# Kernel optimization log

Measured on AMD Instinct MI355X. Metric: run time of the kernel, lower is better.

The kernel has to match this reference:

```python
import jax, jax.numpy as jnp
import numpy as np

# ---------------- config (from ObjectDetector source) ----------------
B = 2; IMG = 224; STRIDE = 32; FH = IMG // STRIDE          # 7x7 feature map
C_FEAT = 1024
SIZES = (32., 64., 128., 256., 512.); RATIOS = (0.5, 1.0, 2.0)
A = len(SIZES) * len(RATIOS)                                # 15 anchors/loc
NA = FH * FH * A                                            # 735 anchors/img
PRE_NMS = min(1000, NA); POST_NMS = min(1000, NA)           # testing config
RPN_NMS_T = 0.7; RPN_MIN_SIZE = 1e-3
NUM_CLASSES = 37
ROI_OUT = 7; ROI_SR = 2; ROI_SCALE = 1.0 / STRIDE
REP = 1024
SCORE_T = 0.05; DET_NMS_T = 0.5; DETS_PER_IMG = 100
CAND_K = 2048            # candidate cap before final batched NMS
MIN_SIZE_DET = 1e-2
BBOX_CLIP = float(np.log(1000.0 / 16.0))


def make_anchors():
    scales = np.array(SIZES, np.float32); ratios = np.array(RATIOS, np.float32)
    h_r = np.sqrt(ratios); w_r = 1.0 / h_r
    ws = (w_r[:, None] * scales[None, :]).reshape(-1)
    hs = (h_r[:, None] * scales[None, :]).reshape(-1)
    base = np.round(np.stack([-ws, -hs, ws, hs], 1) / 2.0)   # [A,4]
    sy, sx = np.meshgrid(np.arange(FH) * STRIDE, np.arange(FH) * STRIDE, indexing='ij')
    shifts = np.stack([sx.reshape(-1), sy.reshape(-1), sx.reshape(-1), sy.reshape(-1)], 1).astype(np.float32)
    return jnp.asarray((shifts[:, None, :] + base[None, :, :]).reshape(-1, 4))  # [NA,4] (H,W,A)


def conv(x, w, b, stride=1, pad=0):
    y = jax.lax.conv_general_dilated(x, w, (stride, stride), [(pad, pad)] * 2,
                                     dimension_numbers=('NCHW', 'OIHW', 'NCHW'))
    return y + b[None, :, None, None]


def decode_boxes(deltas, boxes, weights):
    wx, wy, ww, wh = weights
    w = boxes[..., 2] - boxes[..., 0]; h = boxes[..., 3] - boxes[..., 1]
    cx = boxes[..., 0] + 0.5 * w; cy = boxes[..., 1] + 0.5 * h
    dx = deltas[..., 0] / wx; dy = deltas[..., 1] / wy
    dw = jnp.minimum(deltas[..., 2] / ww, BBOX_CLIP)
    dh = jnp.minimum(deltas[..., 3] / wh, BBOX_CLIP)
    pcx = dx * w + cx; pcy = dy * h + cy
    pw = jnp.exp(dw) * w; ph = jnp.exp(dh) * h
    return jnp.stack([pcx - 0.5 * pw, pcy - 0.5 * ph, pcx + 0.5 * pw, pcy + 0.5 * ph], -1)


def clip_boxes(b):
    x = jnp.clip(b[..., 0::2], 0.0, float(IMG)); y = jnp.clip(b[..., 1::2], 0.0, float(IMG))
    return jnp.stack([x[..., 0], y[..., 0], x[..., 1], y[..., 1]], -1)


def box_iou(a, b):
    area_a = (a[:, 2] - a[:, 0]) * (a[:, 3] - a[:, 1])
    area_b = (b[:, 2] - b[:, 0]) * (b[:, 3] - b[:, 1])
    lt = jnp.maximum(a[:, None, :2], b[None, :, :2])
    rb = jnp.minimum(a[:, None, 2:], b[None, :, 2:])
    wh = jnp.clip(rb - lt, 0.0, None)
    inter = wh[..., 0] * wh[..., 1]
    return inter / jnp.maximum(area_a[:, None] + area_b[None, :] - inter, 1e-9)


def nms_keep(boxes, scores, thresh):
    """Greedy NMS; returns keep mask in original order (fixed shapes)."""
    n = boxes.shape[0]
    order = jnp.argsort(-scores)
    iou = box_iou(*(jax.lax.stop_gradient(boxes[order]),) * 2)
    idx = jnp.arange(n)
    def body(i, keep):
        sup = (iou[i] > thresh) & (idx > i) & keep[i]
        return keep & ~sup
    keep_sorted = jax.lax.fori_loop(0, n, body, jnp.ones(n, bool))
    return jnp.zeros(n, bool).at[order].set(keep_sorted)


def rpn_filter_one(obj_logits, deltas, anchors):
    # obj_logits [NA], deltas [NA,4] (detached, as in torchvision RPN)
    top_v, top_i = jax.lax.top_k(obj_logits, PRE_NMS)
    boxes = clip_boxes(decode_boxes(deltas[top_i], anchors[top_i], (1., 1., 1., 1.)))
    prob = jax.nn.sigmoid(top_v)
    ws = boxes[:, 2] - boxes[:, 0]; hs = boxes[:, 3] - boxes[:, 1]
    prob = jnp.where((ws >= RPN_MIN_SIZE) & (hs >= RPN_MIN_SIZE), prob, -1.0)
    prob = jnp.where(nms_keep(boxes, prob, RPN_NMS_T), prob, -1.0)
    sv, si = jax.lax.top_k(prob, POST_NMS)
    return boxes[si], sv > 0.0


def bilinear(f_hwc, ys, xs):
    # torchvision roi_align bilinear sampling; f_hwc [H,W,C], ys/xs [R,O]
    H, W, _ = f_hwc.shape
    vy = (ys >= -1.0) & (ys <= H); vx = (xs >= -1.0) & (xs <= W)
    y = jnp.clip(ys, 0.0, None); x = jnp.clip(xs, 0.0, None)
    y0 = jnp.minimum(jnp.floor(y).astype(jnp.int32), H - 1)
    x0 = jnp.minimum(jnp.floor(x).astype(jnp.int32), W - 1)
    y1 = jnp.minimum(y0 + 1, H - 1); x1 = jnp.minimum(x0 + 1, W - 1)
    y = jnp.where(y0 == H - 1, y0.astype(y.dtype), y)
    x = jnp.where(x0 == W - 1, x0.astype(x.dtype), x)
    ly = y - y0; lx = x - x0; hy = 1.0 - ly; hx = 1.0 - lx
    g = lambda yi, xi: f_hwc[yi[:, :, None], xi[:, None, :]]   # [R,O,O,C]
    val = ((hy[:, :, None] * hx[:, None, :])[..., None] * g(y0, x0)
         + (hy[:, :, None] * lx[:, None, :])[..., None] * g(y0, x1)
         + (ly[:, :, None] * hx[:, None, :])[..., None] * g(y1, x0)
         + (ly[:, :, None] * lx[:, None, :])[..., None] * g(y1, x1))
    return val * (vy[:, :, None] & vx[:, None, :])[..., None]


def roi_align_one(feat_chw, rois):
    # feat [C,H,W], rois [R,4] -> [R,C,7,7]; output_size=7, sampling_ratio=2, scale=1/32
    f = jnp.transpose(feat_chw, (1, 2, 0))
    x1 = rois[:, 0] * ROI_SCALE; y1 = rois[:, 1] * ROI_SCALE
    rw = jnp.maximum(rois[:, 2] * ROI_SCALE - x1, 1.0)
    rh = jnp.maximum(rois[:, 3] * ROI_SCALE - y1, 1.0)
    bw = rw / ROI_OUT; bh = rh / ROI_OUT
    grid = jnp.arange(ROI_OUT, dtype=jnp.float32)
    acc = 0.0
    for iy in range(ROI_SR):
        ys = y1[:, None] + (grid[None, :] + (iy + 0.5) / ROI_SR) * bh[:, None]
        for ix in range(ROI_SR):
            xs = x1[:, None] + (grid[None, :] + (ix + 0.5) / ROI_SR) * bw[:, None]
            acc = acc + bilinear(f, ys, xs)
    return jnp.transpose(acc / (ROI_SR * ROI_SR), (0, 3, 1, 2))


def postprocess_one(logits, box_deltas, proposals, roi_valid):
    R = logits.shape[0]
    scores = jax.nn.softmax(logits, -1)
    boxes = clip_boxes(decode_boxes(box_deltas.reshape(R, NUM_CLASSES, 4),
                                    proposals[:, None, :], (10., 10., 5., 5.)))
    boxes = boxes[:, 1:, :].reshape(-1, 4)       # drop background class
    scores = jnp.where(roi_valid[:, None], scores[:, 1:], 0.0).reshape(-1)
    labels = jnp.broadcast_to(jnp.arange(1, NUM_CLASSES)[None, :], (R, NUM_CLASSES - 1)).reshape(-1)
    ws = boxes[:, 2] - boxes[:, 0]; hs = boxes[:, 3] - boxes[:, 1]
    ok = (ws >= MIN_SIZE_DET) & (hs >= MIN_SIZE_DET) & (scores > SCORE_T)
    cs, ci = jax.lax.top_k(jnp.where(ok, scores, -1.0), CAND_K)
    cb = boxes[ci]; cl = labels[ci]
    off = cl.astype(cb.dtype) * (IMG + 1.0)      # batched (per-class) NMS trick
    keep = nms_keep(cb + off[:, None], cs, DET_NMS_T)
    tv, ti = jax.lax.top_k(jnp.where(keep, cs, -1.0), DETS_PER_IMG)
    valid = tv > 0.0
    out_boxes = jnp.where(valid[:, None], cb[ti], 0.0)
    out_scores = jnp.where(valid, tv, 0.0)
    out_labels = jnp.where(valid, cl[ti], 0).astype(out_boxes.dtype)
    return jnp.concatenate([out_boxes, out_scores[:, None], out_labels[:, None]], -1)  # [100,6]


def forward(images, params, anchors):
    (bb_w, bb_b, rpn_w, rpn_b, cls_w, cls_b, reg_w, reg_b,
     fc1_w, fc1_b, fc2_w, fc2_b, clsp_w, clsp_b, boxp_w, boxp_b) = params
    Bn = images.shape[0]
    feats = jax.nn.relu(conv(images, bb_w, bb_b, stride=STRIDE))        # [B,1024,7,7]
    t = jax.nn.relu(conv(feats, rpn_w, rpn_b, stride=1, pad=1))
    obj = jnp.transpose(conv(t, cls_w, cls_b), (0, 2, 3, 1)).reshape(Bn, -1)            # [B,NA]
    reg = jnp.transpose(conv(t, reg_w, reg_b).reshape(Bn, A, 4, FH, FH),
                        (0, 3, 4, 1, 2)).reshape(Bn, -1, 4)                              # [B,NA,4]
    obj_d = jax.lax.stop_gradient(obj); reg_d = jax.lax.stop_gradient(reg)  # RPN detaches
    proposals, roi_valid = jax.vmap(lambda o, d: rpn_filter_one(o, d, anchors))(obj_d, reg_d)
    pooled = jax.vmap(roi_align_one)(feats, proposals)                  # [B,R,1024,7,7]
    x = pooled.reshape(Bn * POST_NMS, -1)
    x = jax.nn.relu(x @ fc1_w.T + fc1_b)
    x = jax.nn.relu(x @ fc2_w.T + fc2_b)
    logits = (x @ clsp_w.T + clsp_b).reshape(Bn, POST_NMS, NUM_CLASSES)
    bdelt = (x @ boxp_w.T + boxp_b).reshape(Bn, POST_NMS, NUM_CLASSES * 4)
    return jax.vmap(postprocess_one)(logits, bdelt, proposals, roi_valid)  # [B,100,6]


def setup_inputs() -> dict:
    key = jax.random.key(0)
    ks = jax.random.split(key, 10)
    w = lambda k, shape, s=0.02: jax.random.normal(k, shape, jnp.float32) * s
    return {
        'images': jax.random.uniform(ks[0], (B, 1, IMG, IMG), jnp.float32),
        'bb_w': w(ks[1], (C_FEAT, 1, STRIDE, STRIDE)), 'bb_b': jnp.zeros((C_FEAT,), jnp.float32),
        'rpn_w': w(ks[2], (C_FEAT, C_FEAT, 3, 3)), 'rpn_b': jnp.zeros((C_FEAT,), jnp.float32),
        'cls_w': w(ks[3], (A, C_FEAT, 1, 1)), 'cls_b': jnp.zeros((A,), jnp.float32),
        'reg_w': w(ks[4], (4 * A, C_FEAT, 1, 1)), 'reg_b': jnp.zeros((4 * A,), jnp.float32),
        'fc1_w': w(ks[5], (REP, C_FEAT * ROI_OUT * ROI_OUT), 0.005), 'fc1_b': jnp.zeros((REP,), jnp.float32),
        'fc2_w': w(ks[6], (REP, REP)), 'fc2_b': jnp.zeros((REP,), jnp.float32),
        'clsp_w': w(ks[7], (NUM_CLASSES, REP)), 'clsp_b': jnp.zeros((NUM_CLASSES,), jnp.float32),
        'boxp_w': w(ks[8], (NUM_CLASSES * 4, REP)), 'boxp_b': jnp.zeros((NUM_CLASSES * 4,), jnp.float32),
    }


def reference(images, bb_w, bb_b, rpn_w, rpn_b, cls_w, cls_b, reg_w, reg_b,
              fc1_w, fc1_b, fc2_w, fc2_b, clsp_w, clsp_b, boxp_w, boxp_b):
    anchors = make_anchors()
    params = (bb_w, bb_b, rpn_w, rpn_b, cls_w, cls_b, reg_w, reg_b,
              fc1_w, fc1_b, fc2_w, fc2_b, clsp_w, clsp_b, boxp_w, boxp_b)
    return forward(images, params, anchors)
```

## Files before the change

### kernel.cpp

```cpp
#include <hip/hip_runtime.h>
#include <math.h>

#define NANCH 735
#define NCAND 26460
#define NCANDP 26624
#define BBCLIP 4.135166556742356f
#define KF1 4864
#define KHALF 2432
#define MROW 768
#define MTOT 1536

typedef short bf16x8 __attribute__((ext_vector_type(8)));
typedef float f32x4 __attribute__((ext_vector_type(4)));

__device__ __forceinline__ unsigned short f2b(float f) {
  unsigned int u = __float_as_uint(f);
  unsigned int r = (u >> 16) & 1u;
  u += 0x7fffu + r;
  return (unsigned short)(u >> 16);
}

__device__ __forceinline__ void anchor_of(int i, float* o) {
  int pos = i / 15, a = i % 15;
  int iy = pos / 7, ix = pos % 7;
// ... 1 lines not shown
  double ratio = (rr == 0) ? 0.5 : (rr == 1 ? 1.0 : 2.0);
  double scale = (double)(32 << sc);
  double hr = sqrt(ratio), wr = 1.0 / hr;
  double wsz = wr * scale, hsz = hr * scale;
  float bx1 = (float)rint(-wsz * 0.5), by1 = (float)rint(-hsz * 0.5);
  float bx2 = (float)rint(wsz * 0.5),  by2 = (float)rint(hsz * 0.5);
  float sx = (float)(ix * 32), sy = (float)(iy * 32);
  o[0] = sx + bx1; o[1] = sy + by1; o[2] = sx + bx2; o[3] = sy + by2;
}

__device__ __forceinline__ bool before_(float va, int ia, float vb, int ib) {
  return (va > vb) || (va == vb && ia < ib);
}

template<int NTOT, int NTH>
__device__ void bitonic_sort_sh(float* v, int* id) {
  const int t = threadIdx.x;
  for (int k = 2; k <= NTOT; k <<= 1) {
    for (int j = k >> 1; j > 0; j >>= 1) {
      for (int s = t; s < NTOT; s += NTH) {
        int p = s ^ j;
        if (p > s) {
          float v1 = v[s], v2 = v[p];
          int i1 = id[s], i2 = id[p];
          bool up = ((s & k) == 0);
          if (before_(v2, i2, v1, i1) == up) {
            v[s] = v2; id[s] = i2; v[p] = v1; id[p] = i1;
          }
        }
      }
      __syncthreads();
    }
  }
}

template<int NTOT, int NTH>
__device__ void bitonic_merge_sh(float* v, int* id) {
  const int t = threadIdx.x;
  for (int j = NTOT >> 1; j > 0; j >>= 1) {
    for (int s = t; s < NTOT; s += NTH) {
      int p = s ^ j;
      if (p > s) {
        float v1 = v[s], v2 = v[p];
        int i1 = id[s], i2 = id[p];
        if (before_(v2, i2, v1, i1)) {
          v[s] = v2; id[s] = i2; v[p] = v1; id[p] = i1;
        }
      }
    }
    __syncthreads();
  }
}

__global__ void k_im2col_bb(const float* __restrict__ images, unsigned short* __restrict__ patch) {
  int i = blockIdx.x * 256 + threadIdx.x;
  if (i >= 98 * 1024) return;
  int rowi = i >> 10, k = i & 1023;
  int b = rowi / 49, pos = rowi % 49;
  int oy = pos / 7, ox = pos % 7;
  int ky = k >> 5, kx = k & 31;
  patch[i] = f2b(images[((size_t)b * 224 + oy * 32 + ky) * 224 + ox * 32 + kx]);
}

__global__ void k_im2col_rpn(const unsigned short* __restrict__ bbh,
                             unsigned short* __restrict__ im2) {
  int i = blockIdx.x * 256 + threadIdx.x;
  if (i >= 98 * 9216) return;
  int rowi = i / 9216, k = i % 9216;
  int b = rowi / 49, pos = rowi % 49;
  int oy = pos / 7, ox = pos % 7;
  int ic = k / 9, kk = k % 9;
  int ky = kk / 3, kx = kk % 3;
  int y = oy + ky - 1, x = ox + kx - 1;
  unsigned short v = 0;
  if ((unsigned)y < 7u && (unsigned)x < 7u)
    v = bbh[((size_t)(b * 49 + y * 7 + x)) * 1024 + ic];
  im2[i] = v;
}

__global__ __launch_bounds__(256) void k_gemm_bf16(
    const unsigned short* __restrict__ A, int lda, int M,
    const unsigned short* __restrict__ B, int ldb,
    float* __restrict__ P, int N, int Kchunk,
    const int* __restrict__ nvalid, int Msplit, int boff)
{
  __shared__ __attribute__((aligned(16))) unsigned short As[2][128][40];
  __shared__ __attribute__((aligned(16))) unsigned short Bs[2][128][40];
  const int G = gridDim.x * gridDim.y * gridDim.z;
  int lid = blockIdx.x + gridDim.x * (blockIdx.y + gridDim.y * blockIdx.z);
  lid = (lid & 7) * (G >> 3) + (lid >> 3);
  const int bx = lid % gridDim.x;
  const int rest = lid / gridDim.x;
  const int by = rest % gridDim.y, bz = rest / gridDim.y;
  const int m0 = bx * 128, n0 = by * 128;
  if (nvalid) {
    int img = (Msplit && m0 >= Msplit) ? 1 : 0;
    int lm = m0 - img * Msplit;
    if (lm >= nvalid[img]) return;
    B += (size_t)img * boff;
  }
  const int t = threadIdx.x;
  const int lane = t & 63, wid = t >> 6;
  const int wm = (wid >> 1) * 64, wn = (wid & 1) * 64;
  const size_t k0 = (size_t)bz * Kchunk;
  f32x4 acc[4][4];
#pragma unroll
  for (int i = 0; i < 4; ++i)
#pragma unroll
    for (int j = 0; j < 4; ++j) acc[i][j] = (f32x4){0.f, 0.f, 0.f, 0.f};
  const int r0 = t >> 2, c0 = (t & 3) * 8;
  const int fr = lane & 15, fk = (lane >> 4) * 8;
  const int gmA0 = m0 + r0, gmA1 = m0 + r0 + 64;
  const bool vA0 = gmA0 < M, vA1 = gmA1 < M;
  const unsigned short* pA0 = A + (size_t)gmA0 * lda + k0 + c0;
  const unsigned short* pA1 = A + (size_t)gmA1 * lda + k0 + c0;
  const unsigned short* pB0 = B + (size_t)(n0 + r0) * ldb + k0 + c0;
  const unsigned short* pB1 = B + (size_t)(n0 + r0 + 64) * ldb + k0 + c0;
  bf16x8 rA0 = {}, rA1 = {}, rB0, rB1;
  if (vA0) rA0 = *(const bf16x8*)pA0;
  if (vA1) rA1 = *(const bf16x8*)pA1;
  rB0 = *(const bf16x8*)pB0;
  rB1 = *(const bf16x8*)pB1;
  const int nt = Kchunk >> 5;
  int cur = 0;
  for (int it = 0; it < nt; ++it) {
    *(bf16x8*)&As[cur][r0][c0] = rA0;
    *(bf16x8*)&As[cur][r0 + 64][c0] = rA1;
    *(bf16x8*)&Bs[cur][r0][c0] = rB0;
    *(bf16x8*)&Bs[cur][r0 + 64][c0] = rB1;
    __syncthreads();
    if (it + 1 < nt) {
      size_t ofs = (size_t)(it + 1) * 32;
      rA0 = vA0 ? *(const bf16x8*)(pA0 + ofs) : (bf16x8){};
      rA1 = vA1 ? *(const bf16x8*)(pA1 + ofs) : (bf16x8){};
      rB0 = *(const bf16x8*)(pB0 + ofs);
      rB1 = *(const bf16x8*)(pB1 + ofs);
    }
    bf16x8 af[4], bg[4];
#pragma unroll
    for (int i = 0; i < 4; ++i) af[i] = *(const bf16x8*)&As[cur][wm + i * 16 + fr][fk];
#pragma unroll
    for (int j = 0; j < 4; ++j) bg[j] = *(const bf16x8*)&Bs[cur][wn + j * 16 + fr][fk];
#pragma unroll
    for (int i = 0; i < 4; ++i)
#pragma unroll
      for (int j = 0; j < 4; ++j)
        acc[i][j] = __builtin_amdgcn_mfma_f32_16x16x32_bf16(af[i], bg[j], acc[i][j], 0, 0, 0);
    cur ^= 1;
  }
  float* Pp = P + (size_t)bz * M * N;
#pragma unroll
  for (int i = 0; i < 4; ++i) {
#pragma unroll
    for (int r = 0; r < 4; ++r) {
      int gm = m0 + wm + i * 16 + (lane >> 4) * 4 + r;
      if (gm < M) {
#pragma unroll
        for (int j = 0; j < 4; ++j)
          Pp[(size_t)gm * N + n0 + wn + j * 16 + (lane & 15)] = acc[i][j][r];
      }
    }
  }
}

__global__ __launch_bounds__(256) void k_gemm_mb(
    const unsigned short* __restrict__ A,
    const unsigned short* __restrict__ W1p,
    unsigned short* __restrict__ Bmat)
{
  __shared__ __attribute__((aligned(16))) unsigned short As[2][128][40];
  __shared__ __attribute__((aligned(16))) unsigned short Bs[2][128][40];
  __shared__ unsigned short tile[98][130];
  const int G = gridDim.x * gridDim.y * gridDim.z;
  int lid = blockIdx.x + gridDim.x * (blockIdx.y + gridDim.y * blockIdx.z);
  lid = (lid & 7) * (G >> 3) + (lid >> 3);
  const int rest = lid;
  const int by = rest % gridDim.y, p = rest / gridDim.y;
  const int n0 = by * 128;
  const int M = 98;
  const unsigned short* B = W1p + (size_t)p * 1048576;
  const int t = threadIdx.x;
  const int lane = t & 63, wid = t >> 6;
  const int wm = (wid >> 1) * 64, wn = (wid & 1) * 64;
  f32x4 acc[4][4];
#pragma unroll
  for (int i = 0; i < 4; ++i)
#pragma unroll
    for (int j = 0; j < 4; ++j) acc[i][j] = (f32x4){0.f, 0.f, 0.f, 0.f};
  const int r0 = t >> 2, c0 = (t & 3) * 8;
  const int fr = lane & 15, fk = (lane >> 4) * 8;
  int gA0 = r0; if (gA0 >= M) gA0 = M - 1;
  int gA1 = r0 + 64; if (gA1 >= M) gA1 = M - 1;
  const unsigned short* pA0 = A + (size_t)gA0 * 1024 + c0;
  const unsigned short* pA1 = A + (size_t)gA1 * 1024 + c0;
  const unsigned short* pB0 = B + (size_t)(n0 + r0) * 1024 + c0;
  const unsigned short* pB1 = B + (size_t)(n0 + r0 + 64) * 1024 + c0;
  bf16x8 rA0 = *(const bf16x8*)pA0;
  bf16x8 rA1 = *(const bf16x8*)pA1;
  bf16x8 rB0 = *(const bf16x8*)pB0;
  bf16x8 rB1 = *(const bf16x8*)pB1;
  const int nt = 1024 >> 5;
  int cur = 0;
  for (int it = 0; it < nt; ++it) {
    *(bf16x8*)&As[cur][r0][c0] = rA0;
    *(bf16x8*)&As[cur][r0 + 64][c0] = rA1;
    *(bf16x8*)&Bs[cur][r0][c0] = rB0;
    *(bf16x8*)&Bs[cur][r0 + 64][c0] = rB1;
    __syncthreads();
    if (it + 1 < nt) {
      size_t ofs = (size_t)(it + 1) * 32;
      rA0 = *(const bf16x8*)(pA0 + ofs);
      rA1 = *(const bf16x8*)(pA1 + ofs);
      rB0 = *(const bf16x8*)(pB0 + ofs);
      rB1 = *(const bf16x8*)(pB1 + ofs);
    }
    bf16x8 af[4], bg[4];
#pragma unroll
    for (int i = 0; i < 4; ++i) af[i] = *(const bf16x8*)&As[cur][wm + i * 16 + fr][fk];
#pragma unroll
    for (int j = 0; j < 4; ++j) bg[j] = *(const bf16x8*)&Bs[cur][wn + j * 16 + fr][fk];
#pragma unroll
    for (int i = 0; i < 4; ++i)
#pragma unroll
      for (int j = 0; j < 4; ++j)
        acc[i][j] = __builtin_amdgcn_mfma_f32_16x16x32_bf16(af[i], bg[j], acc[i][j], 0, 0, 0);
    cur ^= 1;
  }
  __syncthreads();
#pragma unroll
  for (int i = 0; i < 4; ++i) {
#pragma unroll
    for (int r = 0; r < 4; ++r) {
      int gm = wm + i * 16 + (lane >> 4) * 4 + r;
      if (gm < M) {
#pragma unroll
        for (int j = 0; j < 4; ++j)
          tile[gm][wn + j * 16 + (lane & 15)] = f2b(acc[i][j][r]);
      }
    }
  }
  __syncthreads();
  {
    int nl = t >> 1, b2 = t & 1;
    unsigned short* dst = Bmat + (size_t)(n0 + nl) * KF1 + b2 * KHALF + p * 49;
    for (int qq = 0; qq < 49; ++qq) dst[qq] = tile[b2 * 49 + qq][nl];
  }
  if (p == 0) {
// ... 16 lines not shown
  int t = threadIdx.x;
  for (int j = t; j < KHALF; j += 256) g[j] = 0.f;
  __syncthreads();
  if (t < 49) {
    int pr = b * NANCH + r; if (pr > 2 * NANCH - 1) pr = 2 * NANCH - 1;
    const float* roi = props + (size_t)pr * 4;
    int p = t, oy = p / 7, ox = p % 7;
    float x1 = roi[0] * 0.03125f, y1 = roi[1] * 0.03125f;
    float rw = fmaxf(roi[2] * 0.03125f - x1, 1.f);
    float rh = fmaxf(roi[3] * 0.03125f - y1, 1.f);
    float bw = rw / 7.f, bh = rh / 7.f;
    float* gb = g + p * 49;
    for (int iy = 0; iy < 2; ++iy) {
      for (int ix = 0; ix < 2; ++ix) {
        float ys = y1 + ((float)oy + ((float)iy + 0.5f) * 0.5f) * bh;
        float xs = x1 + ((float)ox + ((float)ix + 0.5f) * 0.5f) * bw;
        bool vy = (ys >= -1.f) && (ys <= 7.f);
        bool vx = (xs >= -1.f) && (xs <= 7.f);
        float yc = fmaxf(ys, 0.f), xc = fmaxf(xs, 0.f);
        int y0 = min(max((int)floorf(yc), 0), 6), x0 = min(max((int)floorf(xc), 0), 6);
        int y1i = min(y0 + 1, 6), x1i = min(x0 + 1, 6);
        if (y0 == 6) yc = 6.f;
        if (x0 == 6) xc = 6.f;
        float ly = yc - (float)y0, lx = xc - (float)x0;
        float hy = 1.f - ly, hx = 1.f - lx;
        float vm = (vy && vx) ? 0.25f : 0.f;
        gb[y0 * 7 + x0]   += hy * hx * vm;
        gb[y0 * 7 + x1i]  += hy * lx * vm;
        gb[y1i * 7 + x0]  += ly * hx * vm;
        gb[y1i * 7 + x1i] += ly * lx * vm;
      }
    }
  }
  __syncthreads();
  unsigned short* Gr = Gmat + (size_t)rg * KHALF;
  for (int j = t; j < KHALF; j += 256) Gr[j] = f2b(g[j]);
}

__global__ void k_reduce(const float* __restrict__ P, float* __restrict__ dst,
                         unsigned short* __restrict__ dst16,
                         int S, int M, int N, const float* __restrict__ bias, int flags)
{
  size_t i = (size_t)blockIdx.x * 256 + threadIdx.x;
  size_t tot = (size_t)M * N;
  if (i >= tot) return;
  float v = (flags & 1) ? 0.f : dst[i];
  for (int s = 0; s < S; ++s) v += P[(size_t)s * tot + i];
  if (flags & 2) v += bias[i % (size_t)N];
  if (flags & 4) v = fmaxf(v, 0.f);
  if (!(flags & 16)) dst[i] = v;
  if (flags & 8) dst16[i] = f2b(v);
}

__global__ void k_f2b3(const float* __restrict__ s1, unsigned short* __restrict__ d1,
                       const float* __restrict__ s2, unsigned short* __restrict__ d2,
                       const float* __restrict__ s3, unsigned short* __restrict__ d3,
                       const float* __restrict__ cw, const float* __restrict__ bw,
                       unsigned short* __restrict__ d4)
{
  int i = (blockIdx.x * 256 + threadIdx.x) * 4;
  const float* s; unsigned short* d; int off;
  if (i < 1048576) { s = s1; d = d1; off = i; }
  else if (i < 2097152) { s = s2; d = d2; off = i - 1048576; }
  else if (i < 11534336) { s = s3; d = d3; off = i - 2097152; }
  else if (i < 11796480) {
    int off4 = i - 11534336;
    int row = off4 >> 10, col = off4 & 1023;
    ushort4 o;
    if (row < 37) {
      float4 v = *(const float4*)(cw + (size_t)row * 1024 + col);
      o.x = f2b(v.x); o.y = f2b(v.y); o.z = f2b(v.z); o.w = f2b(v.w);
    } else if (row < 185) {
      float4 v = *(const float4*)(bw + (size_t)(row - 37) * 1024 + col);
      o.x = f2b(v.x); o.y = f2b(v.y); o.z = f2b(v.z); o.w = f2b(v.w);
    } else {
      o.x = 0; o.y = 0; o.z = 0; o.w = 0;
    }
    *(ushort4*)(d4 + off4) = o;
    return;
  }
  else return;
  float4 v = *(const float4*)(s + off);
  ushort4 o;
  o.x = f2b(v.x); o.y = f2b(v.y); o.z = f2b(v.z); o.w = f2b(v.w);
  *(ushort4*)(d + off) = o;
}

__global__ __launch_bounds__(256) void k_w1perm2(const float* __restrict__ w,
                                                 unsigned short* __restrict__ o)
{
  __shared__ unsigned short tile[128 * 50];
  const int n = blockIdx.x, ct = blockIdx.y;
  const float* src = w + (size_t)n * 50176 + (size_t)ct * 128 * 49;
  const int t = threadIdx.x;
  for (int i = t; i < 6272; i += 256) {
    int cl = i / 49, p = i % 49;
    tile[cl * 50 + p] = f2b(src[i]);
  }
  __syncthreads();
  for (int j = t; j < 6272; j += 256) {
    int p = j >> 7, cl = j & 127;
    o[((size_t)p * 1024 + n) * 1024 + (size_t)ct * 128 + cl] = tile[cl * 50 + p];
  }
}

__global__ __launch_bounds__(256) void k_rpn_head(
    const float* __restrict__ tmn, const float* __restrict__ cls_w,
    const float* __restrict__ cls_b, const float* __restrict__ reg_w,
    const float* __restrict__ reg_b, float* __restrict__ obj, float* __restrict__ reg)
{
  int blk = blockIdx.x;
  __shared__ float col[1024];
  const float* row = tmn + (size_t)blk * 1024;
  for (int i = threadIdx.x; i < 1024; i += 256) col[i] = row[i];
  __syncthreads();
  int b = blk / 49, pos = blk % 49;
  for (int o = threadIdx.x; o < 75; o += 256) {
    const float* w = (o < 15) ? (cls_w + (size_t)o * 1024) : (reg_w + (size_t)(o - 15) * 1024);
    float s = 0.f;
    for (int k = 0; k < 1024; ++k) s = fmaf(col[k], w[k], s);
    if (o < 15) {
      obj[(size_t)b * NANCH + pos * 15 + o] = s + cls_b[o];
    } else {
      int c = o - 15, a = c >> 2, d = c & 3;
      reg[((size_t)b * NANCH + pos * 15 + a) * 4 + d] = s + reg_b[c];
    }
  }
}

__global__ __launch_bounds__(1024) void k_rpn_prep(
    const float* __restrict__ obj, const float* __restrict__ reg,
    float* __restrict__ bxp, float* __restrict__ pnms)
{
#pragma clang fp contract(off)
  const int b = blockIdx.x, t = threadIdx.x;
  __shared__ float sval[1024];
  __shared__ float vo1[1024];
  __shared__ int o1a[1024];
  __shared__ int wtv[16];
  __shared__ int wti[16];
  sval[t] = (t < NANCH) ? obj[(size_t)b * NANCH + t] : -INFINITY;
  __syncthreads();
  {
    float v = sval[t];
    int rank = 0;
    for (int j = 0; j < NANCH; ++j) {
      float u = sval[j];
      rank += (u > v) || (u == v && j < t);
    }
    if (t < NANCH) { vo1[rank] = v; o1a[rank] = t; }
  }
  __syncthreads();
  float x1 = 0.f, y1 = 0.f, x2 = 0.f, y2 = 0.f, prob = -1.f;
  bool flag = false;
  if (t < NANCH) {
    int ai = o1a[t];
    const float* d = reg + ((size_t)b * NANCH + ai) * 4;
    float an[4];
// ... 59 lines not shown
    float iw = fmaxf(ix2 - ix1, 0.f), ih = fmaxf(iy2 - iy1, 0.f);
    float inter = iw * ih;
    float iou = inter / fmaxf(aarea + barea - inter, 1e-9f);
    if (iou > 0.7f) bits |= 1ull << (l & 63);
  }
  rmask[((size_t)b * NANCH + row) * 12 + w] = bits;
}

__global__ __launch_bounds__(1024) void k_rpn_fin(
    const float* __restrict__ bxp, const float* __restrict__ pnms,
    const unsigned long long* __restrict__ rmask,
    float* __restrict__ props, int* __restrict__ meta)
{
  const int b = blockIdx.x, t = threadIdx.x;
  __shared__ unsigned long long smask[NANCH * 12];
  __shared__ float sp[1024];
  __shared__ unsigned long long keepw[12];
  __shared__ int wtot[16];
  for (int i = t; i < NANCH * 12; i += 1024)
    smask[i] = rmask[(size_t)b * NANCH * 12 + i];
  sp[t] = (t < NANCH) ? pnms[(size_t)b * NANCH + t] : -1.f;
  __syncthreads();
  if (t < 64) {
    unsigned long long kl = (t < 12) ? ~0ull : 0ull;
    for (int i = 0; i < NANCH; ++i) {
      unsigned long long kw = __shfl(kl, i >> 6);
      unsigned long long m = (t < 12) ? smask[i * 12 + t] : 0ull;
      bool on = (kw >> (i & 63)) & 1ull;
      kl &= on ? ~m : ~0ull;
    }
    if (t < 12) keepw[t] = kl;
  }
  __syncthreads();
  bool flag = false;
  if (t < NANCH) {
    bool kp = (keepw[t >> 6] >> (t & 63)) & 1ull;
    flag = kp && (sp[t] > 0.f);
  }
  unsigned long long bal = __ballot(flag);
  int lane = t & 63, w = t >> 6;
  if (lane == 0) wtot[w] = __popcll(bal);
  __syncthreads();
  int base = 0, tot = 0;
  for (int k = 0; k < 16; ++k) { int c = wtot[k]; if (k < w) base += c; tot += c; }
  if (flag) {
    int pos = base + __popcll(bal & ((1ull << lane) - 1));
    const float* src = bxp + ((size_t)b * NANCH + t) * 4;
    float* o = props + ((size_t)b * NANCH + pos) * 4;
    o[0] = src[0]; o[1] = src[1]; o[2] = src[2]; o[3] = src[3];
  }
  if (t == 0) meta[b] = tot;
}

__global__ void k_cand(const float* __restrict__ P, const float* __restrict__ cb_,
                       const float* __restrict__ bb_, const float* __restrict__ props,
                       const int* __restrict__ meta,
                       float* __restrict__ cscore, float* __restrict__ cbox)
{
#pragma clang fp contract(off)
  int rg = blockIdx.x * blockDim.x + threadIdx.x;
  if (rg >= 2 * NANCH) return;
  int b = rg / NANCH, r = rg % NANCH;
  float* cs = cscore + (size_t)b * NCANDP;
  float* cbx = cbox + (size_t)b * NCANDP * 4;
  int base = r * 36;
  if (r >= meta[b]) {
    for (int j = 0; j < 36; ++j) {
      cs[base + j] = -1.f;
      float* q = cbx + (size_t)(base + j) * 4;
      q[0] = 0.f; q[1] = 0.f; q[2] = 0.f; q[3] = 0.f;
    }
    return;
  }
  int row = b * MROW + r;
  const float* p0 = P + (size_t)row * 256;
  const float* p1 = P + (size_t)MTOT * 256 + (size_t)row * 256;
  float lg[37];
  for (int c = 0; c < 37; ++c) lg[c] = p0[c] + p1[c] + cb_[c];
  float mx = lg[0];
  for (int c = 1; c < 37; ++c) mx = fmaxf(mx, lg[c]);
  float sum = 0.f;
  for (int c = 0; c < 37; ++c) sum += expf(lg[c] - mx);
  const float* roi = props + (size_t)rg * 4;
  float rw = roi[2] - roi[0], rh = roi[3] - roi[1];
  float rcx = roi[0] + 0.5f * rw, rcy = roi[1] + 0.5f * rh;
  for (int c = 1; c < 37; ++c) {
    float d0 = p0[37 + c * 4]     + p1[37 + c * 4]     + bb_[c * 4];
    float d1 = p0[37 + c * 4 + 1] + p1[37 + c * 4 + 1] + bb_[c * 4 + 1];
    float d2 = p0[37 + c * 4 + 2] + p1[37 + c * 4 + 2] + bb_[c * 4 + 2];
    float d3 = p0[37 + c * 4 + 3] + p1[37 + c * 4 + 3] + bb_[c * 4 + 3];
    float dx = d0 / 10.f, dy = d1 / 10.f;
    float dw = fminf(d2 / 5.f, BBCLIP), dh = fminf(d3 / 5.f, BBCLIP);
    float pcx = dx * rw + rcx, pcy = dy * rh + rcy;
    float pw = expf(dw) * rw, ph = expf(dh) * rh;
    float x1 = pcx - 0.5f * pw, y1 = pcy - 0.5f * ph;
    float x2 = pcx + 0.5f * pw, y2 = pcy + 0.5f * ph;
    x1 = fminf(fmaxf(x1, 0.f), 224.f);
    y1 = fminf(fmaxf(y1, 0.f), 224.f);
    x2 = fminf(fmaxf(x2, 0.f), 224.f);
    y2 = fminf(fmaxf(y2, 0.f), 224.f);
    float sc = expf(lg[c] - mx) / sum;
    bool ok = ((x2 - x1) >= 1e-2f) && ((y2 - y1) >= 1e-2f) && (sc > 0.05f);
    cs[base + c - 1] = ok ? sc : -1.f;
    float* q = cbx + (size_t)(base + c - 1) * 4;
    q[0] = x1; q[1] = y1; q[2] = x2; q[3] = y2;
  }
}

__global__ __launch_bounds__(1024) void k_top2048(
    const float* __restrict__ cscore,
    float* __restrict__ sel_score, int* __restrict__ sel_cidx,
    int* __restrict__ meta)
{
  const int b = blockIdx.x, t = threadIdx.x;
  __shared__ float Lv[2048]; __shared__ int Li[2048];
  __shared__ float Cv[2048]; __shared__ int Ci[2048];
  __shared__ int cnt;
  const float* cs = cscore + (size_t)b * NCANDP;
  if (t == 0) cnt = 0;
  __syncthreads();
  for (int gi = t; gi < NCAND; gi += 1024) {
    float v = cs[gi];
    if (v > 0.f) {
      int p = atomicAdd(&cnt, 1);
      if (p < 2048) { Cv[p] = v; Ci[p] = gi; }
    }
  }
  __syncthreads();
  int npos = cnt;
  if (npos <= 2048) {
    for (int h = 0; h < 2; ++h) {
      int p = h * 1024 + t;
      if (p < npos) {
        float v = Cv[p]; int id = Ci[p];
        int rank = 0;
        for (int j = 0; j < npos; ++j) {
          float u = Cv[j]; int ju = Ci[j];
          rank += (u > v) || (u == v && ju < id);
        }
        sel_score[b * 2048 + rank] = v;
        sel_cidx[b * 2048 + rank] = id;
      }
      if (p >= npos && p < 2048) {
        sel_score[b * 2048 + p] = -1.f;
        sel_cidx[b * 2048 + p] = 0;
      }
    }
    if (t == 0) meta[2 + b] = npos;
    return;
  }
  for (int chunk = 0; chunk < 13; ++chunk) {
    for (int s = t; s < 2048; s += 1024) {
      int gi = chunk * 2048 + s;
      Cv[s] = (gi < NCAND) ? cs[gi] : -INFINITY;
      Ci[s] = gi;
    }
    __syncthreads();
    bitonic_sort_sh<2048, 1024>(Cv, Ci);
    if (chunk == 0) {
      for (int s = t; s < 2048; s += 1024) { Lv[s] = Cv[s]; Li[s] = Ci[s]; }
      __syncthreads();
    } else {
      for (int s = t; s < 2048; s += 1024) {
        float cv = Cv[2047 - s]; int ci = Ci[2047 - s];
        if (before_(cv, ci, Lv[s], Li[s])) { Lv[s] = cv; Li[s] = ci; }
      }
      __syncthreads();
      bitonic_merge_sh<2048, 1024>(Lv, Li);
    }
  }
  for (int s = t; s < 2048; s += 1024) {
    sel_score[b * 2048 + s] = Lv[s];
    sel_cidx[b * 2048 + s] = Li[s];
  }
  if (t == 0) meta[2 + b] = 2048;
}

__global__ void k_detmask(const int* __restrict__ sel_cidx,
                          const float* __restrict__ cbox,
                          const int* __restrict__ meta,
                          unsigned long long* __restrict__ dmask)
{
#pragma clang fp contract(off)
  int blk = blockIdx.x;
  int b = blk >> 8, row0 = (blk & 255) * 8;
  int npos = meta[2 + b];
  if (row0 >= npos) return;
  int t = threadIdx.x;
  int i = row0 + (t >> 5), w = t & 31;
  if (i >= npos) return;
  int ci = sel_cidx[b * 2048 + i];
  const float* bp = cbox + ((size_t)b * NCANDP + ci) * 4;
  float off = (float)(ci % 36 + 1) * 225.f;
  float a0 = bp[0] + off, a1 = bp[1] + off, a2 = bp[2] + off, a3 = bp[3] + off;
  float aarea = (a2 - a0) * (a3 - a1);
  unsigned long long bits = 0ull;
  int l0 = w * 64;
  int l1 = (l0 + 64 < npos) ? l0 + 64 : npos;
  int ls = (l0 > i + 1) ? l0 : i + 1;
  for (int l = ls; l < l1; ++l) {
    int cl = sel_cidx[b * 2048 + l];
    const float* q = cbox + ((size_t)b * NCANDP + cl) * 4;
    float o2 = (float)(cl % 36 + 1) * 225.f;
    float b0 = q[0] + o2, b1 = q[1] + o2, b2 = q[2] + o2, b3 = q[3] + o2;
    float barea = (b2 - b0) * (b3 - b1);
    float ix1 = fmaxf(a0, b0), iy1 = fmaxf(a1, b1);
    float ix2 = fminf(a2, b2), iy2 = fminf(a3, b3);
    float iw = fmaxf(ix2 - ix1, 0.f), ih = fmaxf(iy2 - iy1, 0.f);
    float inter = iw * ih;
    float iou = inter / fmaxf(aarea + barea - inter, 1e-9f);
    if (iou > 0.5f) bits |= 1ull << (l & 63);
  }
  dmask[((size_t)b * 2048 + i) * 32 + w] = bits;
}

__global__ __launch_bounds__(1024) void k_final(
    const float* __restrict__ sel_score, const int* __restrict__ sel_cidx,
    const float* __restrict__ cbox, const unsigned long long* __restrict__ dmask,
    const int* __restrict__ meta, float* __restrict__ out)
{
  const int b = blockIdx.x, t = threadIdx.x;
  __shared__ unsigned long long keepw[32];
  __shared__ float sv[2048];
  __shared__ float kv[2048]; __shared__ int ks[2048];
  __shared__ int wtot[32];
  int npos = meta[2 + b];
  for (int h = 0; h < 2; ++h) {
    int s = h * 1024 + t;
// ... 98 lines not shown
  size_t o_reg   = alloc(1470ull * 16);
  size_t o_props = alloc(1470ull * 16);
  size_t o_bxp   = alloc(1470ull * 16);
  size_t o_pnms  = alloc(1470ull * 4);
  size_t o_rm    = alloc(1470ull * 12 * 8);
  size_t o_meta  = alloc(256);
  size_t o_y1    = alloc((size_t)MTOT * 1024 * 4);
  size_t o_cs    = alloc(2ull * NCANDP * 4);
  size_t o_cb    = alloc(2ull * NCANDP * 16);
  size_t o_ss    = alloc(2ull * 2048 * 4);
  size_t o_sc    = alloc(2ull * 2048 * 4);
  size_t o_dm    = alloc(2ull * 2048 * 32 * 8);
  size_t o_w0b   = alloc(1048576ull * 2);
  size_t o_w3b   = alloc(9437184ull * 2);
  size_t o_w1p   = alloc(51380224ull * 2);
  size_t o_bmat  = alloc(1024ull * KF1 * 2);
  size_t o_gmat  = alloc((size_t)MTOT * KHALF * 2);
  size_t o_w2b   = alloc(1048576ull * 2);
  size_t o_hwb   = alloc(256ull * 1024 * 2);
  size_t o_y1b   = alloc((size_t)MTOT * 1024 * 2);
  size_t o_y2b   = alloc((size_t)MTOT * 1024 * 2);
  size_t o_P     = alloc(32ull * 98 * 1024 * 4 > 2ull * MTOT * 1024 * 4
                         ? 32ull * 98 * 1024 * 4 : 2ull * MTOT * 1024 * 4);

  unsigned short* patchb = (unsigned short*)(ws + o_patch);
  float* bbC   = (float*)(ws + o_bbC);
  unsigned short* bbh = (unsigned short*)(ws + o_bbh);
  float* tb    = (float*)(ws + o_t);
  unsigned short* im2b = (unsigned short*)(ws + o_im2);
  float* objb  = (float*)(ws + o_obj);
  float* regb  = (float*)(ws + o_reg);
  float* props = (float*)(ws + o_props);
  float* bxp   = (float*)(ws + o_bxp);
  float* pnms  = (float*)(ws + o_pnms);
  unsigned long long* rmb = (unsigned long long*)(ws + o_rm);
  int*   meta  = (int*)(ws + o_meta);
  float* y1    = (float*)(ws + o_y1);
  float* csb   = (float*)(ws + o_cs);
  float* cbb   = (float*)(ws + o_cb);
  float* ssb   = (float*)(ws + o_ss);
  int*   scb   = (int*)(ws + o_sc);
  unsigned long long* dmb = (unsigned long long*)(ws + o_dm);
  unsigned short* w0b = (unsigned short*)(ws + o_w0b);
  unsigned short* w3b = (unsigned short*)(ws + o_w3b);
  unsigned short* w1p = (unsigned short*)(ws + o_w1p);
  unsigned short* bmat = (unsigned short*)(ws + o_bmat);
  unsigned short* gmat = (unsigned short*)(ws + o_gmat);
  unsigned short* w2b = (unsigned short*)(ws + o_w2b);
  unsigned short* hwb = (unsigned short*)(ws + o_hwb);
  unsigned short* y1b = (unsigned short*)(ws + o_y1b);
  unsigned short* y2b = (unsigned short*)(ws + o_y2b);
  float* Pb    = (float*)(ws + o_P);

  k_w1perm2<<<dim3(1024, 8), 256, 0, stream>>>(fc1_w, w1p);
  k_f2b3<<<11520, 256, 0, stream>>>(fc2_w, w2b, bb_w, w0b, rpn_w, w3b, clsp_w, boxp_w, hwb);
  k_im2col_bb<<<392, 256, 0, stream>>>(images, patchb);
  k_gemm_bf16<<<dim3(1, 8, 8), 256, 0, stream>>>(patchb, 1024, 98, w0b, 1024, Pb, 1024, 128, nullptr, 0, 0);
  k_reduce<<<392, 256, 0, stream>>>(Pb, bbC, bbh, 8, 98, 1024, bb_b, 31);
  k_gemm_mb<<<dim3(1, 8, 49), 256, 0, stream>>>(bbh, w1p, bmat);
  k_im2col_rpn<<<3528, 256, 0, stream>>>(bbh, im2b);
  k_gemm_bf16<<<dim3(1, 8, 32), 256, 0, stream>>>(im2b, 9216, 98, w3b, 9216, Pb, 1024, 288, nullptr, 0, 0);
  k_reduce<<<392, 256, 0, stream>>>(Pb, tb, nullptr, 32, 98, 1024, rpn_b, 7);
  k_rpn_head<<<98, 256, 0, stream>>>(tb, cls_w, cls_b, reg_w, reg_b, objb, regb);
  k_rpn_prep<<<2, 1024, 0, stream>>>(objb, regb, bxp, pnms);
  k_rpn_mask<<<70, 256, 0, stream>>>(bxp, rmb);
  k_rpn_fin<<<2, 1024, 0, stream>>>(bxp, pnms, rmb, props, meta);
  k_gbuild<<<MTOT, 256, 0, stream>>>(props, gmat);
  k_gemm_bf16<<<dim3(12, 8, 2), 256, 0, stream>>>(gmat, KHALF, MTOT, bmat, KF1, Pb, 1024, 1216, meta, MROW, KHALF);
  k_reduce<<<6144, 256, 0, stream>>>(Pb, y1, y1b, 2, MTOT, 1024, fc1_b, 31);
  k_gemm_bf16<<<dim3(12, 8, 2), 256, 0, stream>>>(y1b, 1024, MTOT, w2b, 1024, Pb, 1024, 512, meta, MROW, 0);
  k_reduce<<<6144, 256, 0, stream>>>(Pb, y1, y2b, 2, MTOT, 1024, fc2_b, 31);
  k_gemm_bf16<<<dim3(12, 2, 2), 256, 0, stream>>>(y2b, 1024, MTOT, hwb, 1024, Pb, 256, 512, meta, MROW, 0);
  k_cand<<<6, 256, 0, stream>>>(Pb, clsp_b, boxp_b, props, meta, csb, cbb);
  k_top2048<<<2, 1024, 0, stream>>>(csb, ssb, scb, meta);
  k_detmask<<<512, 256, 0, stream>>>(scb, cbb, meta, dmb);
  k_final<<<2, 1024, 0, stream>>>(ssb, scb, cbb, dmb, meta, out);
}
```

Before: 447.9 us.

## Fuse preprocessing, im2col with fc1 reshuffle GEMM, and candidate scoring with top-k

Three groups of adjacent launches are merged into single kernels that branch on block index. The weight bf16 conversion, the backbone im2col and the fc1 permutation become one launch, k_pre. The RPN im2col and the fc1 weight-mixing GEMM become one launch, and candidate decoding is folded into the per-image top-2048 kernel. The aim is to cut launch and inter-kernel gap overhead; the merged candidate stage now runs on only two 1024-thread blocks instead of six 256-thread blocks.

```diff
diff --git a/kernel.cpp b/kernel.cpp
--- a/kernel.cpp
+++ b/kernel.cpp
@@ -77,30 +77,71 @@
   }
 }
 
-__global__ void k_im2col_bb(const float* __restrict__ images, unsigned short* __restrict__ patch) {
-  int i = blockIdx.x * 256 + threadIdx.x;
-  if (i >= 98 * 1024) return;
-  int rowi = i >> 10, k = i & 1023;
-  int b = rowi / 49, pos = rowi % 49;
-  int oy = pos / 7, ox = pos % 7;
-  int ky = k >> 5, kx = k & 31;
-  patch[i] = f2b(images[((size_t)b * 224 + oy * 32 + ky) * 224 + ox * 32 + kx]);
-}
-
-__global__ void k_im2col_rpn(const unsigned short* __restrict__ bbh,
-                             unsigned short* __restrict__ im2) {
-  int i = blockIdx.x * 256 + threadIdx.x;
-  if (i >= 98 * 9216) return;
-  int rowi = i / 9216, k = i % 9216;
-  int b = rowi / 49, pos = rowi % 49;
-  int oy = pos / 7, ox = pos % 7;
-  int ic = k / 9, kk = k % 9;
-  int ky = kk / 3, kx = kk % 3;
-  int y = oy + ky - 1, x = ox + kx - 1;
-  unsigned short v = 0;
-  if ((unsigned)y < 7u && (unsigned)x < 7u)
-    v = bbh[((size_t)(b * 49 + y * 7 + x)) * 1024 + ic];
-  im2[i] = v;
+__global__ __launch_bounds__(256) void k_pre(
+    const float* __restrict__ fc2_w, unsigned short* __restrict__ w2b,
+    const float* __restrict__ bb_w, unsigned short* __restrict__ w0b,
+    const float* __restrict__ rpn_w, unsigned short* __restrict__ w3b,
+    const float* __restrict__ cw, const float* __restrict__ bw,
+    unsigned short* __restrict__ hwb,
+    const float* __restrict__ images, unsigned short* __restrict__ patch,
+    const float* __restrict__ fc1_w, unsigned short* __restrict__ w1p)
+{
+  __shared__ unsigned short tile[128 * 50];
+  int blk = blockIdx.x;
+  const int t = threadIdx.x;
+  if (blk < 11520) {
+    int i = (blk * 256 + t) * 4;
+    const float* s; unsigned short* d; int off;
+    if (i < 1048576) { s = fc2_w; d = w2b; off = i; }
+    else if (i < 2097152) { s = bb_w; d = w0b; off = i - 1048576; }
+    else if (i < 11534336) { s = rpn_w; d = w3b; off = i - 2097152; }
+    else {
+      int off4 = i - 11534336;
+      int row = off4 >> 10, col = off4 & 1023;
+      ushort4 o;
+      if (row < 37) {
+        float4 v = *(const float4*)(cw + (size_t)row * 1024 + col);
+        o.x = f2b(v.x); o.y = f2b(v.y); o.z = f2b(v.z); o.w = f2b(v.w);
+      } else if (row < 185) {
+        float4 v = *(const float4*)(bw + (size_t)(row - 37) * 1024 + col);
+        o.x = f2b(v.x); o.y = f2b(v.y); o.z = f2b(v.z); o.w = f2b(v.w);
+      } else {
+        o.x = 0; o.y = 0; o.z = 0; o.w = 0;
+      }
+      *(ushort4*)(hwb + off4) = o;
+      return;
+    }
+    float4 v = *(const float4*)(s + off);
+    ushort4 o;
+    o.x = f2b(v.x); o.y = f2b(v.y); o.z = f2b(v.z); o.w = f2b(v.w);
+    *(ushort4*)(d + off) = o;
+    return;
+  }
+  blk -= 11520;
+  if (blk < 392) {
+    int i = blk * 256 + t;
+    if (i >= 98 * 1024) return;
+    int rowi = i >> 10, k = i & 1023;
+    int b = rowi / 49, pos = rowi % 49;
+    int oy = pos / 7, ox = pos % 7;
+    int ky = k >> 5, kx = k & 31;
+    patch[i] = f2b(images[((size_t)b * 224 + oy * 32 + ky) * 224 + ox * 32 + kx]);
+    return;
+  }
+  blk -= 392;
+  {
+    const int n = blk >> 3, ct = blk & 7;
+    const float* src = fc1_w + (size_t)n * 50176 + (size_t)ct * 128 * 49;
+    for (int i = t; i < 6272; i += 256) {
+      int cl = i / 49, p = i % 49;
+      tile[cl * 50 + p] = f2b(src[i]);
+    }
+    __syncthreads();
+    for (int j = t; j < 6272; j += 256) {
+      int p = j >> 7, cl = j & 127;
+      w1p[((size_t)p * 1024 + n) * 1024 + (size_t)ct * 128 + cl] = tile[cl * 50 + p];
+    }
+  }
 }
 
 __global__ __launch_bounds__(256) void k_gemm_bf16(
@@ -188,23 +229,38 @@
   }
 }
 
-__global__ __launch_bounds__(256) void k_gemm_mb(
-    const unsigned short* __restrict__ A,
+__global__ __launch_bounds__(256) void k_imrpn_mb(
+    const unsigned short* __restrict__ bbh,
+    unsigned short* __restrict__ im2,
     const unsigned short* __restrict__ W1p,
     unsigned short* __restrict__ Bmat)
 {
   __shared__ __attribute__((aligned(16))) unsigned short As[2][128][40];
   __shared__ __attribute__((aligned(16))) unsigned short Bs[2][128][40];
   __shared__ unsigned short tile[98][130];
-  const int G = gridDim.x * gridDim.y * gridDim.z;
-  int lid = blockIdx.x + gridDim.x * (blockIdx.y + gridDim.y * blockIdx.z);
-  lid = (lid & 7) * (G >> 3) + (lid >> 3);
-  const int rest = lid;
-  const int by = rest % gridDim.y, p = rest / gridDim.y;
+  const int t = threadIdx.x;
+  int blk = blockIdx.x;
+  if (blk < 3528) {
+    int i = blk * 256 + t;
+    if (i >= 98 * 9216) return;
+    int rowi = i / 9216, k = i % 9216;
+    int b = rowi / 49, pos = rowi % 49;
+    int oy = pos / 7, ox = pos % 7;
+    int ic = k / 9, kk = k % 9;
+    int ky = kk / 3, kx = kk % 3;
+    int y = oy + ky - 1, x = ox + kx - 1;
+    unsigned short v = 0;
+    if ((unsigned)y < 7u && (unsigned)x < 7u)
+      v = bbh[((size_t)(b * 49 + y * 7 + x)) * 1024 + ic];
+    im2[i] = v;
+    return;
+  }
+  int lid = blk - 3528;
+  lid = (lid & 7) * 49 + (lid >> 3);
+  const int by = lid % 8, p = lid / 8;
   const int n0 = by * 128;
   const int M = 98;
   const unsigned short* B = W1p + (size_t)p * 1048576;
-  const int t = threadIdx.x;
   const int lane = t & 63, wid = t >> 6;
   const int wm = (wid >> 1) * 64, wn = (wid & 1) * 64;
   f32x4 acc[4][4];
@@ -216,8 +272,8 @@
   const int fr = lane & 15, fk = (lane >> 4) * 8;
   int gA0 = r0; if (gA0 >= M) gA0 = M - 1;
   int gA1 = r0 + 64; if (gA1 >= M) gA1 = M - 1;
-  const unsigned short* pA0 = A + (size_t)gA0 * 1024 + c0;
-  const unsigned short* pA1 = A + (size_t)gA1 * 1024 + c0;
+  const unsigned short* pA0 = bbh + (size_t)gA0 * 1024 + c0;
+  const unsigned short* pA1 = bbh + (size_t)gA1 * 1024 + c0;
   const unsigned short* pB0 = B + (size_t)(n0 + r0) * 1024 + c0;
   const unsigned short* pB1 = B + (size_t)(n0 + r0 + 64) * 1024 + c0;
   bf16x8 rA0 = *(const bf16x8*)pA0;
@@ -340,58 +396,6 @@
   if (flags & 8) dst16[i] = f2b(v);
 }
 
-__global__ void k_f2b3(const float* __restrict__ s1, unsigned short* __restrict__ d1,
-                       const float* __restrict__ s2, unsigned short* __restrict__ d2,
-                       const float* __restrict__ s3, unsigned short* __restrict__ d3,
-                       const float* __restrict__ cw, const float* __restrict__ bw,
-                       unsigned short* __restrict__ d4)
-{
-  int i = (blockIdx.x * 256 + threadIdx.x) * 4;
-  const float* s; unsigned short* d; int off;
-  if (i < 1048576) { s = s1; d = d1; off = i; }
-  else if (i < 2097152) { s = s2; d = d2; off = i - 1048576; }
-  else if (i < 11534336) { s = s3; d = d3; off = i - 2097152; }
-  else if (i < 11796480) {
-    int off4 = i - 11534336;
-    int row = off4 >> 10, col = off4 & 1023;
-    ushort4 o;
-    if (row < 37) {
-      float4 v = *(const float4*)(cw + (size_t)row * 1024 + col);
-      o.x = f2b(v.x); o.y = f2b(v.y); o.z = f2b(v.z); o.w = f2b(v.w);
-    } else if (row < 185) {
-      float4 v = *(const float4*)(bw + (size_t)(row - 37) * 1024 + col);
-      o.x = f2b(v.x); o.y = f2b(v.y); o.z = f2b(v.z); o.w = f2b(v.w);
-    } else {
-      o.x = 0; o.y = 0; o.z = 0; o.w = 0;
-    }
-    *(ushort4*)(d4 + off4) = o;
-    return;
-  }
-  else return;
-  float4 v = *(const float4*)(s + off);
-  ushort4 o;
-  o.x = f2b(v.x); o.y = f2b(v.y); o.z = f2b(v.z); o.w = f2b(v.w);
-  *(ushort4*)(d + off) = o;
-}
-
-__global__ __launch_bounds__(256) void k_w1perm2(const float* __restrict__ w,
-                                                 unsigned short* __restrict__ o)
-{
-  __shared__ unsigned short tile[128 * 50];
-  const int n = blockIdx.x, ct = blockIdx.y;
-  const float* src = w + (size_t)n * 50176 + (size_t)ct * 128 * 49;
-  const int t = threadIdx.x;
-  for (int i = t; i < 6272; i += 256) {
-    int cl = i / 49, p = i % 49;
-    tile[cl * 50 + p] = f2b(src[i]);
-  }
-  __syncthreads();
-  for (int j = t; j < 6272; j += 256) {
-    int p = j >> 7, cl = j & 127;
-    o[((size_t)p * 1024 + n) * 1024 + (size_t)ct * 128 + cl] = tile[cl * 50 + p];
-  }
-}
-
 __global__ __launch_bounds__(256) void k_rpn_head(
     const float* __restrict__ tmn, const float* __restrict__ cls_w,
     const float* __restrict__ cls_b, const float* __restrict__ reg_w,
@@ -557,71 +561,69 @@
   if (t == 0) meta[b] = tot;
 }
 
-__global__ void k_cand(const float* __restrict__ P, const float* __restrict__ cb_,
-                       const float* __restrict__ bb_, const float* __restrict__ props,
-                       const int* __restrict__ meta,
-                       float* __restrict__ cscore, float* __restrict__ cbox)
+__global__ __launch_bounds__(1024) void k_candtop(
+    const float* __restrict__ P, const float* __restrict__ cb_,
+    const float* __restrict__ bb_, const float* __restrict__ props,
+    const int* __restrict__ meta,
+    float* __restrict__ cscore, float* __restrict__ cbox,
+    float* __restrict__ sel_score, int* __restrict__ sel_cidx,
+    int* __restrict__ metao)
 {
 #pragma clang fp contract(off)
-  int rg = blockIdx.x * blockDim.x + threadIdx.x;
-  if (rg >= 2 * NANCH) return;
-  int b = rg / NANCH, r = rg % NANCH;
-  float* cs = cscore + (size_t)b * NCANDP;
-  float* cbx = cbox + (size_t)b * NCANDP * 4;
-  int base = r * 36;
-  if (r >= meta[b]) {
-    for (int j = 0; j < 36; ++j) {
-      cs[base + j] = -1.f;
-      float* q = cbx + (size_t)(base + j) * 4;
-      q[0] = 0.f; q[1] = 0.f; q[2] = 0.f; q[3] = 0.f;
-    }
-    return;
-  }
-  int row = b * MROW + r;
-  const float* p0 = P + (size_t)row * 256;
-  const float* p1 = P + (size_t)MTOT * 256 + (size_t)row * 256;
-  float lg[37];
-  for (int c = 0; c < 37; ++c) lg[c] = p0[c] + p1[c] + cb_[c];
-  float mx = lg[0];
-  for (int c = 1; c < 37; ++c) mx = fmaxf(mx, lg[c]);
-  float sum = 0.f;
-  for (int c = 0; c < 37; ++c) sum += expf(lg[c] - mx);
-  const float* roi = props + (size_t)rg * 4;
-  float rw = roi[2] - roi[0], rh = roi[3] - roi[1];
-  float rcx = roi[0] + 0.5f * rw, rcy = roi[1] + 0.5f * rh;
-  for (int c = 1; c < 37; ++c) {
-    float d0 = p0[37 + c * 4]     + p1[37 + c * 4]     + bb_[c * 4];
-    float d1 = p0[37 + c * 4 + 1] + p1[37 + c * 4 + 1] + bb_[c * 4 + 1];
-    float d2 = p0[37 + c * 4 + 2] + p1[37 + c * 4 + 2] + bb_[c * 4 + 2];
-    float d3 = p0[37 + c * 4 + 3] + p1[37 + c * 4 + 3] + bb_[c * 4 + 3];
-    float dx = d0 / 10.f, dy = d1 / 10.f;
-    float dw = fminf(d2 / 5.f, BBCLIP), dh = fminf(d3 / 5.f, BBCLIP);
-    float pcx = dx * rw + rcx, pcy = dy * rh + rcy;
-    float pw = expf(dw) * rw, ph = expf(dh) * rh;
-    float x1 = pcx - 0.5f * pw, y1 = pcy - 0.5f * ph;
-    float x2 = pcx + 0.5f * pw, y2 = pcy + 0.5f * ph;
-    x1 = fminf(fmaxf(x1, 0.f), 224.f);
-    y1 = fminf(fmaxf(y1, 0.f), 224.f);
-    x2 = fminf(fmaxf(x2, 0.f), 224.f);
-    y2 = fminf(fmaxf(y2, 0.f), 224.f);
-    float sc = expf(lg[c] - mx) / sum;
-    bool ok = ((x2 - x1) >= 1e-2f) && ((y2 - y1) >= 1e-2f) && (sc > 0.05f);
-    cs[base + c - 1] = ok ? sc : -1.f;
-    float* q = cbx + (size_t)(base + c - 1) * 4;
-    q[0] = x1; q[1] = y1; q[2] = x2; q[3] = y2;
-  }
-}
-
-__global__ __launch_bounds__(1024) void k_top2048(
-    const float* __restrict__ cscore,
-    float* __restrict__ sel_score, int* __restrict__ sel_cidx,
-    int* __restrict__ meta)
-{
   const int b = blockIdx.x, t = threadIdx.x;
   __shared__ float Lv[2048]; __shared__ int Li[2048];
   __shared__ float Cv[2048]; __shared__ int Ci[2048];
   __shared__ int cnt;
-  const float* cs = cscore + (size_t)b * NCANDP;
+  float* cs = cscore + (size_t)b * NCANDP;
+  float* cbx = cbox + (size_t)b * NCANDP * 4;
+  {
+    int nv = meta[b];
+    for (int r = t; r < NANCH; r += 1024) {
+      int base = r * 36;
+      if (r >= nv) {
+        for (int j = 0; j < 36; ++j) {
+          cs[base + j] = -1.f;
+          float* q = cbx + (size_t)(base + j) * 4;
+          q[0] = 0.f; q[1] = 0.f; q[2] = 0.f; q[3] = 0.f;
+        }
+        continue;
+      }
+      int row = b * MROW + r;
+      const float* p0 = P + (size_t)row * 256;
+      const float* p1 = P + (size_t)MTOT * 256 + (size_t)row * 256;
+      float lg[37];
+      for (int c = 0; c < 37; ++c) lg[c] = p0[c] + p1[c] + cb_[c];
+      float mx = lg[0];
+      for (int c = 1; c < 37; ++c) mx = fmaxf(mx, lg[c]);
+      float sum = 0.f;
+      for (int c = 0; c < 37; ++c) sum += expf(lg[c] - mx);
+      int rg = b * NANCH + r;
+      const float* roi = props + (size_t)rg * 4;
+      float rw = roi[2] - roi[0], rh = roi[3] - roi[1];
+      float rcx = roi[0] + 0.5f * rw, rcy = roi[1] + 0.5f * rh;
+      for (int c = 1; c < 37; ++c) {
+        float d0 = p0[37 + c * 4]     + p1[37 + c * 4]     + bb_[c * 4];
+        float d1 = p0[37 + c * 4 + 1] + p1[37 + c * 4 + 1] + bb_[c * 4 + 1];
+        float d2 = p0[37 + c * 4 + 2] + p1[37 + c * 4 + 2] + bb_[c * 4 + 2];
+        float d3 = p0[37 + c * 4 + 3] + p1[37 + c * 4 + 3] + bb_[c * 4 + 3];
+        float dx = d0 / 10.f, dy = d1 / 10.f;
+        float dw = fminf(d2 / 5.f, BBCLIP), dh = fminf(d3 / 5.f, BBCLIP);
+        float pcx = dx * rw + rcx, pcy = dy * rh + rcy;
+        float pw = expf(dw) * rw, ph = expf(dh) * rh;
+        float x1 = pcx - 0.5f * pw, y1 = pcy - 0.5f * ph;
+        float x2 = pcx + 0.5f * pw, y2 = pcy + 0.5f * ph;
+        x1 = fminf(fmaxf(x1, 0.f), 224.f);
+        y1 = fminf(fmaxf(y1, 0.f), 224.f);
+        x2 = fminf(fmaxf(x2, 0.f), 224.f);
+        y2 = fminf(fmaxf(y2, 0.f), 224.f);
+        float sc = expf(lg[c] - mx) / sum;
+        bool ok = ((x2 - x1) >= 1e-2f) && ((y2 - y1) >= 1e-2f) && (sc > 0.05f);
+        cs[base + c - 1] = ok ? sc : -1.f;
+        float* q = cbx + (size_t)(base + c - 1) * 4;
+        q[0] = x1; q[1] = y1; q[2] = x2; q[3] = y2;
+      }
+    }
+  }
   if (t == 0) cnt = 0;
   __syncthreads();
   for (int gi = t; gi < NCAND; gi += 1024) {
@@ -651,7 +653,7 @@
         sel_cidx[b * 2048 + p] = 0;
       }
     }
-    if (t == 0) meta[2 + b] = npos;
+    if (t == 0) metao[2 + b] = npos;
     return;
   }
   for (int chunk = 0; chunk < 13; ++chunk) {
@@ -678,7 +680,7 @@
     sel_score[b * 2048 + s] = Lv[s];
     sel_cidx[b * 2048 + s] = Li[s];
   }
-  if (t == 0) meta[2 + b] = 2048;
+  if (t == 0) metao[2 + b] = 2048;
 }
 
 __global__ void k_detmask(const int* __restrict__ sel_cidx,
@@ -883,13 +885,11 @@
   unsigned short* y2b = (unsigned short*)(ws + o_y2b);
   float* Pb    = (float*)(ws + o_P);
 
-  k_w1perm2<<<dim3(1024, 8), 256, 0, stream>>>(fc1_w, w1p);
-  k_f2b3<<<11520, 256, 0, stream>>>(fc2_w, w2b, bb_w, w0b, rpn_w, w3b, clsp_w, boxp_w, hwb);
-  k_im2col_bb<<<392, 256, 0, stream>>>(images, patchb);
+  k_pre<<<20104, 256, 0, stream>>>(fc2_w, w2b, bb_w, w0b, rpn_w, w3b,
+                                   clsp_w, boxp_w, hwb, images, patchb, fc1_w, w1p);
   k_gemm_bf16<<<dim3(1, 8, 8), 256, 0, stream>>>(patchb, 1024, 98, w0b, 1024, Pb, 1024, 128, nullptr, 0, 0);
   k_reduce<<<392, 256, 0, stream>>>(Pb, bbC, bbh, 8, 98, 1024, bb_b, 31);
-  k_gemm_mb<<<dim3(1, 8, 49), 256, 0, stream>>>(bbh, w1p, bmat);
-  k_im2col_rpn<<<3528, 256, 0, stream>>>(bbh, im2b);
+  k_imrpn_mb<<<3920, 256, 0, stream>>>(bbh, im2b, w1p, bmat);
   k_gemm_bf16<<<dim3(1, 8, 32), 256, 0, stream>>>(im2b, 9216, 98, w3b, 9216, Pb, 1024, 288, nullptr, 0, 0);
   k_reduce<<<392, 256, 0, stream>>>(Pb, tb, nullptr, 32, 98, 1024, rpn_b, 7);
   k_rpn_head<<<98, 256, 0, stream>>>(tb, cls_w, cls_b, reg_w, reg_b, objb, regb);
@@ -902,8 +902,7 @@
   k_gemm_bf16<<<dim3(12, 8, 2), 256, 0, stream>>>(y1b, 1024, MTOT, w2b, 1024, Pb, 1024, 512, meta, MROW, 0);
   k_reduce<<<6144, 256, 0, stream>>>(Pb, y1, y2b, 2, MTOT, 1024, fc2_b, 31);
   k_gemm_bf16<<<dim3(12, 2, 2), 256, 0, stream>>>(y2b, 1024, MTOT, hwb, 1024, Pb, 256, 512, meta, MROW, 0);
-  k_cand<<<6, 256, 0, stream>>>(Pb, clsp_b, boxp_b, props, meta, csb, cbb);
-  k_top2048<<<2, 1024, 0, stream>>>(csb, ssb, scb, meta);
+  k_candtop<<<2, 1024, 0, stream>>>(Pb, clsp_b, boxp_b, props, meta, csb, cbb, ssb, scb, meta);
   k_detmask<<<512, 256, 0, stream>>>(scb, cbb, meta, dmb);
   k_final<<<2, 1024, 0, stream>>>(ssb, scb, cbb, dmb, meta, out);
 }
```

Result: slower. 517.9 us (+15.6%).
